# Performance work log

Hardware: AMD Instinct MI355X
Metric: run time of the kernel (lower is better)

Reference implementation:

```python
import jax, jax.numpy as jnp
import numpy as np

EPS = 1e-6

def rms_norm(x):
    # x / sqrt(mean(x^2, axis=-1) + eps)
    return x * jax.lax.rsqrt(jnp.mean(x * x, axis=-1, keepdims=True) + EPS)

def setup_inputs() -> dict:
    key = jax.random.key(0)
    k1, k2, k3 = jax.random.split(key, 3)
    T, B, D = 2048, 16, 1024
    x = jax.random.normal(k1, (T, B, D), dtype=jnp.float32)
    h0 = jax.random.normal(k2, (B, D), dtype=jnp.float32)
    # Orthogonal-ish init scaled by 0.5 (faithful to nn.init.orthogonal_ then *0.5)
    A = jax.random.normal(k3, (D, D), dtype=jnp.float32)
    Q, _ = jnp.linalg.qr(A)
    W = 0.5 * Q
    b = jnp.zeros((D,), dtype=jnp.float32)
    log_alpha = jnp.asarray(np.log(0.1), dtype=jnp.float32)
    return {"x": x, "h0": h0, "W": W, "b": b, "log_alpha": log_alpha}

def reference(x, h0, W, b, log_alpha):
    T, B, D = x.shape
    alpha = jnp.exp(log_alpha)
    # Precompute Wx for all timesteps: [T, B, D]
    Wx_all = jnp.einsum('tbd,ed->tbe', x, W) + b

    def step(h_prev, wx_t):
        h_raw = h_prev + alpha * wx_t
        h_new = rms_norm(h_raw)
        out = h_new * jax.nn.silu(h_new)
        return h_new, (h_new, out)

    _, (h_seq, output) = jax.lax.scan(step, h0, Wx_all)
    h = jnp.concatenate([h0[None], h_seq], axis=0)  # [T+1, B, D]
    return output, h
```

## Files before the change

### kernel.cpp

```cpp
#include <hip/hip_runtime.h>
#include <hip/hip_bf16.h>

#define TT 2048
#define BB 16
#define DD 1024
#define BD (BB*DD)
#define MR (TT*BB)
#define EPSV 1e-6f
#define INVD (1.0f/1024.0f)
#define CH 256
#define NCH (TT/CH)
#define RING 8

typedef __bf16 bf16x8_t __attribute__((ext_vector_type(8)));
typedef float  f32x4_t  __attribute__((ext_vector_type(4)));
typedef __attribute__((address_space(1))) void gvoid_t;
typedef __attribute__((address_space(3))) void lvoid_t;

static __device__ __forceinline__ float wave_red_sum(float ss) {
    asm volatile(
        "s_nop 1\n\t"
        "v_add_f32 %0, %0, %0 row_shr:1 bound_ctrl:0\n\t"
        "s_nop 1\n\t"
        "v_add_f32 %0, %0, %0 row_shr:2 bound_ctrl:0\n\t"
        "s_nop 1\n\t"
        "v_add_f32 %0, %0, %0 row_shr:4 bank_mask:0xe\n\t"
        "s_nop 1\n\t"
        "v_add_f32 %0, %0, %0 row_shr:8 bank_mask:0xc\n\t"
        "s_nop 1\n\t"
        "v_add_f32 %0, %0, %0 row_bcast:15 row_mask:0xa\n\t"
        "s_nop 1\n\t"
        "v_add_f32 %0, %0, %0 row_bcast:31 row_mask:0xc\n\t"
        "s_nop 1"
        : "+v"(ss));
    return __builtin_bit_cast(float, __builtin_amdgcn_readlane(__builtin_bit_cast(int, ss), 63));
}

static __device__ __forceinline__ unsigned short f2bf(float f) {
    __hip_bfloat16 h = __float2bfloat16(f);
    return __builtin_bit_cast(unsigned short, h);
}

__global__ void k_convert(const float* __restrict__ x, const float* __restrict__ W,
                          unsigned short* __restrict__ xb, unsigned short* __restrict__ wb) {
    const long NX4 = (long)MR * DD / 4;
    const long NW4 = (long)DD * DD / 4;
    const long stride = (long)gridDim.x * blockDim.x;
    for (long j = (long)blockIdx.x * blockDim.x + threadIdx.x; j < NX4 + NW4; j += stride) {
        const float4* src; unsigned short* dst; long o;
        if (j < NX4) { src = (const float4*)x; dst = xb; o = j; }
        else         { src = (const float4*)W; dst = wb; o = j - NX4; }
        float4 v = src[o];
        ushort4 u;
        u.x = f2bf(v.x); u.y = f2bf(v.y); u.z = f2bf(v.z); u.w = f2bf(v.w);
        *(ushort4*)(dst + o * 4) = u;
    }
}

__global__ __launch_bounds__(256, 2)
void k_gemm(const unsigned short* __restrict__ A, const unsigned short* __restrict__ Bw,
            const float* __restrict__ bias, float* __restrict__ C) {
    __shared__ char lds[16384];
    char* ldsA = lds;
    char* ldsB = lds + 8192;
    const int tid  = threadIdx.x;
    const int lane = tid & 63;
    const int wid  = tid >> 6;
    const int wm = wid >> 1, wn = wid & 1;
    const size_t arow0 = (size_t)blockIdx.y * 128;
    const int    brow0 = blockIdx.x * 128;

    f32x4_t acc[4][4] = {};

    const int off0 = tid * 16,        row0_ = off0 >> 6, colb0 = off0 & 63;
    const int off1 = 4096 + tid * 16, row1_ = off1 >> 6, colb1 = off1 & 63;

    for (int kk = 0; kk < DD / 32; ++kk) {
        const int kbase = kk * 32;
        __builtin_amdgcn_global_load_lds(
            (gvoid_t*)(A + (arow0 + row0_) * DD + kbase + (colb0 >> 1)),
            (lvoid_t*)(ldsA + off0), 16, 0, 0);
        __builtin_amdgcn_global_load_lds(
            (gvoid_t*)(A + (arow0 + row1_) * DD + kbase + (colb1 >> 1)),
            (lvoid_t*)(ldsA + off1), 16, 0, 0);
        __builtin_amdgcn_global_load_lds(
            (gvoid_t*)(Bw + (size_t)(brow0 + row0_) * DD + kbase + (colb0 >> 1)),
            (lvoid_t*)(ldsB + off0), 16, 0, 0);
        __builtin_amdgcn_global_load_lds(
            (gvoid_t*)(Bw + (size_t)(brow0 + row1_) * DD + kbase + (colb1 >> 1)),
            (lvoid_t*)(ldsB + off1), 16, 0, 0);
        __syncthreads();

        const int ml = lane & 15;
        const int kh = (lane >> 4) * 16;
        bf16x8_t av[4], bv[4];
        #pragma unroll
        for (int i = 0; i < 4; ++i) {
            av[i] = *(const bf16x8_t*)(ldsA + (wm * 64 + i * 16 + ml) * 64 + kh);
            bv[i] = *(const bf16x8_t*)(ldsB + (wn * 64 + i * 16 + ml) * 64 + kh);
        }
        #pragma unroll
        for (int i = 0; i < 4; ++i)
            #pragma unroll
            for (int j = 0; j < 4; ++j)
                acc[i][j] = __builtin_amdgcn_mfma_f32_16x16x32_bf16(av[i], bv[j], acc[i][j], 0, 0, 0);
        __syncthreads();
    }

    const int rq = (lane >> 4) * 4;
    const int cl = lane & 15;
    #pragma unroll
    for (int i = 0; i < 4; ++i) {
        #pragma unroll
        for (int j = 0; j < 4; ++j) {
            const int n = brow0 + wn * 64 + j * 16 + cl;
            const float bb = bias[n];
            #pragma unroll
            for (int q = 0; q < 4; ++q) {
                const size_t m = arow0 + wm * 64 + i * 16 + rq + q;
                C[m * DD + n] = acc[i][j][q] + bb;
            }
        }
    }
}

__global__ __launch_bounds__(64, 1)
void k_phaseA(const float* __restrict__ Wx, const float* __restrict__ h0,
              const float* __restrict__ la, float* __restrict__ hout,
              float* __restrict__ rtab) {
    const int b = blockIdx.x;
    const int lane = threadIdx.x;
    const int dof = lane * 4;
    const float alpha = expf(la[0]);
    const float* wbase = Wx + b * DD + dof;

    float h[16];
    #pragma unroll
    for (int k = 0; k < 4; ++k) {
        float4 v = *(const float4*)(h0 + b * DD + k * 256 + dof);
        h[k*4+0] = v.x; h[k*4+1] = v.y; h[k*4+2] = v.z; h[k*4+3] = v.w;
    }
    asm volatile("" :: "v"(h[0]), "v"(h[1]), "v"(h[2]), "v"(h[3]),
                       "v"(h[4]), "v"(h[5]), "v"(h[6]), "v"(h[7]),
                       "v"(h[8]), "v"(h[9]), "v"(h[10]), "v"(h[11]),
                       "v"(h[12]), "v"(h[13]), "v"(h[14]), "v"(h[15]));
    __builtin_amdgcn_sched_barrier(0);

    f32x4_t buf[RING][4];
    #pragma unroll
    for (int s = 0; s < RING; ++s) {
        const float* wp = wbase + (size_t)s * BD;
        #pragma unroll
        for (int k = 0; k < 4; ++k)
            asm volatile("global_load_dwordx4 %0, %1, off"
                         : "=v"(buf[s][k]) : "v"(wp + k * 256));
    }

    float r_keep = 0.f;

    for (int tt = 0; tt < TT; tt += 8) {
        #pragma unroll
        for (int g = 0; g < 2; ++g) {
            const int m0 = tt + g * 4;

            asm volatile("s_waitcnt vmcnt(16)" ::: "memory");
            __builtin_amdgcn_sched_barrier(0);

            if ((m0 & 255) == 0) {
                float* hp = hout + (size_t)m0 * BD + b * DD;
                #pragma unroll
                for (int k = 0; k < 4; ++k) {
                    float4 v; v.x = h[k*4+0]; v.y = h[k*4+1];
                    v.z = h[k*4+2]; v.w = h[k*4+3];
                    *(float4*)(hp + k * 256 + dof) = v;
                }
            }

            #pragma unroll
            for (int s4 = 0; s4 < 4; ++s4) {
                const int s = g * 4 + s4;
                const int m = m0 + s4;
                float hr[16];
                float p0 = 0.f, p1 = 0.f, p2 = 0.f, p3 = 0.f;
                #pragma unroll
                for (int k = 0; k < 4; ++k) {
                    const f32x4_t w = buf[s][k];
                    hr[k*4+0] = fmaf(alpha, w[0], h[k*4+0]);
                    hr[k*4+1] = fmaf(alpha, w[1], h[k*4+1]);
                    hr[k*4+2] = fmaf(alpha, w[2], h[k*4+2]);
                    hr[k*4+3] = fmaf(alpha, w[3], h[k*4+3]);
                    p0 = fmaf(hr[k*4+0], hr[k*4+0], p0);
                    p1 = fmaf(hr[k*4+1], hr[k*4+1], p1);
                    p2 = fmaf(hr[k*4+2], hr[k*4+2], p2);
                    p3 = fmaf(hr[k*4+3], hr[k*4+3], p3);
                }
                const float total = wave_red_sum((p0 + p1) + (p2 + p3));
                const float rt = __builtin_amdgcn_rsqf(fmaf(total, INVD, EPSV));
                r_keep = (lane == (m & 63)) ? rt : r_keep;
                #pragma unroll
                for (int e = 0; e < 16; ++e) h[e] = rt * hr[e];
            }

            if (g == 1 && (tt & 63) == 56)
                rtab[(size_t)b * TT + (tt - 56) + lane] = r_keep;

            #pragma unroll
            for (int s4 = 0; s4 < 4; ++s4) {
                const int s = g * 4 + s4;
                const float* wp = wbase + (size_t)((m0 + 8 + s4) & (TT - 1)) * BD;
                #pragma unroll
                for (int k = 0; k < 4; ++k)
                    asm volatile("global_load_dwordx4 %0, %1, off"
                                 : "=v"(buf[s][k]) : "v"(wp + k * 256));
            }
        }
    }

    asm volatile("s_waitcnt vmcnt(0)" ::: "memory");
}

__global__ __launch_bounds__(256)
void k_phaseB(float* __restrict__ WxOut, float* __restrict__ hout,
              const float* __restrict__ rtab, const float* __restrict__ la) {
    const int col = blockIdx.x * 256 + threadIdx.x;
    const int c = blockIdx.y;
    const int b = col >> 10;
    const float alpha = expf(la[0]);
    const float* rr = rtab + b * TT;
    float h = hout[(size_t)(c * CH) * BD + col];
    const int t0 = c * CH + 1;
    float w = WxOut[(size_t)(t0 - 1) * BD + col];
    for (int s = 0; s < CH; ++s) {
        const int t = t0 + s;
        float wnext = 0.f;
        if (s + 1 < CH) wnext = WxOut[(size_t)t * BD + col];
        const float r = rr[t - 1];
        const float hraw = fmaf(alpha, w, h);
        const float hn = r * hraw;
        const float sg = 1.0f / (1.0f + __expf(-hn));
        WxOut[(size_t)(t - 1) * BD + col] = hn * hn * sg;
        if ((t & (CH - 1)) != 0 || t == TT)
            hout[(size_t)t * BD + col] = hn;
        h = hn;
        w = wnext;
    }
}

extern "C" void kernel_launch(void* const* d_in, const int* in_sizes, int n_in,
                              void* d_out, int out_size, void* d_ws, size_t ws_size,
                              hipStream_t stream) {
    (void)in_sizes; (void)n_in; (void)out_size; (void)ws_size;
    const float* x    = (const float*)d_in[0];
    const float* h0   = (const float*)d_in[1];
    const float* W    = (const float*)d_in[2];
    const float* bias = (const float*)d_in[3];
    const float* la   = (const float*)d_in[4];

    float* outr = (float*)d_out;
    float* hreg = outr + (size_t)TT * BD;
    unsigned short* xb = (unsigned short*)hreg;
    unsigned short* wb = xb + (size_t)MR * DD;
    float* rtab = (float*)d_ws;

    k_convert<<<2048, 256, 0, stream>>>(x, W, xb, wb);
    k_gemm<<<dim3(DD / 128, MR / 128), 256, 0, stream>>>(xb, wb, bias, outr);
    k_phaseA<<<BB, 64, 0, stream>>>(outr, h0, la, hreg, rtab);
    k_phaseB<<<dim3(BD / 256, NCH), 256, 0, stream>>>(outr, hreg, rtab, la);
}
```

Measured before the change: 512.4 us.

## Fuse GEMM, sequential scan and output pass into one persistent kernel with counters

Combines the GEMM, the per-batch sequential RMS-norm scan and the chunked output pass into a single launch whose blocks pick roles by block id. Atomic row-tile counters let the scan start as soon as the GEMM rows it needs are written, and per-batch progress flags let output chunks start while the scan continues. The scan and early GEMM tiles get raised wave priority. This adds spin-waits and relies on all scan blocks being resident and making forward progress, and it moves the bf16 staging buffers so they do not overlap the live h region.

Result: slower. 880.3 us (+71.8%).

```diff
diff --git a/kernel.cpp b/kernel.cpp
--- a/kernel.cpp
+++ b/kernel.cpp
@@ -11,6 +11,10 @@
 #define CH 256
 #define NCH (TT/CH)
 #define RING 8
+
+#define ID_GEMM   16
+#define ID_PB     2064
+#define ID_END    2576
 
 typedef __bf16 bf16x8_t __attribute__((ext_vector_type(8)));
 typedef float  f32x4_t  __attribute__((ext_vector_type(4)));
@@ -58,198 +62,237 @@
 }
 
 __global__ __launch_bounds__(256, 2)
-void k_gemm(const unsigned short* __restrict__ A, const unsigned short* __restrict__ Bw,
-            const float* __restrict__ bias, float* __restrict__ C) {
+void k_mega(const unsigned short* __restrict__ A, const unsigned short* __restrict__ Bw,
+            const float* __restrict__ bias, float* __restrict__ outr,
+            const float* __restrict__ h0, const float* __restrict__ la,
+            float* __restrict__ hreg, float* __restrict__ rtab,
+            int* cnt, int* prog, int role_base, int gated) {
     __shared__ char lds[16384];
-    char* ldsA = lds;
-    char* ldsB = lds + 8192;
-    const int tid  = threadIdx.x;
-    const int lane = tid & 63;
-    const int wid  = tid >> 6;
-    const int wm = wid >> 1, wn = wid & 1;
-    const size_t arow0 = (size_t)blockIdx.y * 128;
-    const int    brow0 = blockIdx.x * 128;
-
-    f32x4_t acc[4][4] = {};
-
-    const int off0 = tid * 16,        row0_ = off0 >> 6, colb0 = off0 & 63;
-    const int off1 = 4096 + tid * 16, row1_ = off1 >> 6, colb1 = off1 & 63;
-
-    for (int kk = 0; kk < DD / 32; ++kk) {
-        const int kbase = kk * 32;
-        __builtin_amdgcn_global_load_lds(
-            (gvoid_t*)(A + (arow0 + row0_) * DD + kbase + (colb0 >> 1)),
-            (lvoid_t*)(ldsA + off0), 16, 0, 0);
-        __builtin_amdgcn_global_load_lds(
-            (gvoid_t*)(A + (arow0 + row1_) * DD + kbase + (colb1 >> 1)),
-            (lvoid_t*)(ldsA + off1), 16, 0, 0);
-        __builtin_amdgcn_global_load_lds(
-            (gvoid_t*)(Bw + (size_t)(brow0 + row0_) * DD + kbase + (colb0 >> 1)),
-            (lvoid_t*)(ldsB + off0), 16, 0, 0);
-        __builtin_amdgcn_global_load_lds(
-            (gvoid_t*)(Bw + (size_t)(brow0 + row1_) * DD + kbase + (colb1 >> 1)),
-            (lvoid_t*)(ldsB + off1), 16, 0, 0);
-        __syncthreads();
-
-        const int ml = lane & 15;
-        const int kh = (lane >> 4) * 16;
-        bf16x8_t av[4], bv[4];
+    const int id = blockIdx.x + role_base;
+    const int tid = threadIdx.x;
+
+    if (id >= ID_GEMM && id < ID_PB) {
+        const int gid = id - ID_GEMM;
+        const int gx = gid & 7, gy = gid >> 3;
+        if (gated && gy < 64) __builtin_amdgcn_s_setprio(1);
+        char* ldsA = lds;
+        char* ldsB = lds + 8192;
+        const int lane = tid & 63;
+        const int wid  = tid >> 6;
+        const int wm = wid >> 1, wn = wid & 1;
+        const size_t arow0 = (size_t)gy * 128;
+        const int    brow0 = gx * 128;
+
+        f32x4_t acc[4][4] = {};
+        const int off0 = tid * 16,        row0_ = off0 >> 6, colb0 = off0 & 63;
+        const int off1 = 4096 + tid * 16, row1_ = off1 >> 6, colb1 = off1 & 63;
+
+        for (int kk = 0; kk < DD / 32; ++kk) {
+            const int kbase = kk * 32;
+            __builtin_amdgcn_global_load_lds(
+                (gvoid_t*)(A + (arow0 + row0_) * DD + kbase + (colb0 >> 1)),
+                (lvoid_t*)(ldsA + off0), 16, 0, 0);
+            __builtin_amdgcn_global_load_lds(
+                (gvoid_t*)(A + (arow0 + row1_) * DD + kbase + (colb1 >> 1)),
+                (lvoid_t*)(ldsA + off1), 16, 0, 0);
+            __builtin_amdgcn_global_load_lds(
+                (gvoid_t*)(Bw + (size_t)(brow0 + row0_) * DD + kbase + (colb0 >> 1)),
+                (lvoid_t*)(ldsB + off0), 16, 0, 0);
+            __builtin_amdgcn_global_load_lds(
+                (gvoid_t*)(Bw + (size_t)(brow0 + row1_) * DD + kbase + (colb1 >> 1)),
+                (lvoid_t*)(ldsB + off1), 16, 0, 0);
+            __syncthreads();
+
+            const int ml = lane & 15;
+            const int kh = (lane >> 4) * 16;
+            bf16x8_t av[4], bv[4];
+            #pragma unroll
+            for (int i = 0; i < 4; ++i) {
+                av[i] = *(const bf16x8_t*)(ldsA + (wm * 64 + i * 16 + ml) * 64 + kh);
+                bv[i] = *(const bf16x8_t*)(ldsB + (wn * 64 + i * 16 + ml) * 64 + kh);
+            }
+            #pragma unroll
+            for (int i = 0; i < 4; ++i)
+                #pragma unroll
+                for (int j = 0; j < 4; ++j)
+                    acc[i][j] = __builtin_amdgcn_mfma_f32_16x16x32_bf16(av[i], bv[j], acc[i][j], 0, 0, 0);
+            __syncthreads();
+        }
+
+        const int rq = (lane >> 4) * 4;
+        const int cl = lane & 15;
         #pragma unroll
         for (int i = 0; i < 4; ++i) {
-            av[i] = *(const bf16x8_t*)(ldsA + (wm * 64 + i * 16 + ml) * 64 + kh);
-            bv[i] = *(const bf16x8_t*)(ldsB + (wn * 64 + i * 16 + ml) * 64 + kh);
-        }
+            #pragma unroll
+            for (int j = 0; j < 4; ++j) {
+                const int n = brow0 + wn * 64 + j * 16 + cl;
+                const float bb = bias[n];
+                #pragma unroll
+                for (int q = 0; q < 4; ++q) {
+                    const size_t m = arow0 + wm * 64 + i * 16 + rq + q;
+                    outr[m * DD + n] = acc[i][j][q] + bb;
+                }
+            }
+        }
+        if (gated) {
+            __syncthreads();
+            if (tid == 0)
+                __hip_atomic_fetch_add(&cnt[gy], 1, __ATOMIC_RELEASE,
+                                       __HIP_MEMORY_SCOPE_AGENT);
+        }
+        return;
+    }
+
+    if (id < ID_GEMM) {
+        const int b = id;
+        if (tid >= 64) return;
+        const int lane = tid;
+        const int dof = lane * 4;
+        const float alpha = expf(la[0]);
+        const float* wbase = outr + b * DD + dof;
+        __builtin_amdgcn_s_setprio(1);
+
+        float h[16];
         #pragma unroll
-        for (int i = 0; i < 4; ++i)
-            #pragma unroll
-            for (int j = 0; j < 4; ++j)
-                acc[i][j] = __builtin_amdgcn_mfma_f32_16x16x32_bf16(av[i], bv[j], acc[i][j], 0, 0, 0);
-        __syncthreads();
-    }
-
-    const int rq = (lane >> 4) * 4;
-    const int cl = lane & 15;
-    #pragma unroll
-    for (int i = 0; i < 4; ++i) {
+        for (int k = 0; k < 4; ++k) {
+            float4 v = *(const float4*)(h0 + b * DD + k * 256 + dof);
+            h[k*4+0] = v.x; h[k*4+1] = v.y; h[k*4+2] = v.z; h[k*4+3] = v.w;
+        }
+        asm volatile("" :: "v"(h[0]), "v"(h[1]), "v"(h[2]), "v"(h[3]),
+                           "v"(h[4]), "v"(h[5]), "v"(h[6]), "v"(h[7]),
+                           "v"(h[8]), "v"(h[9]), "v"(h[10]), "v"(h[11]),
+                           "v"(h[12]), "v"(h[13]), "v"(h[14]), "v"(h[15]));
+        __builtin_amdgcn_sched_barrier(0);
+
+        if (gated && lane == 0) {
+            while (__hip_atomic_load(&cnt[0], __ATOMIC_ACQUIRE,
+                                     __HIP_MEMORY_SCOPE_AGENT) < 8)
+                __builtin_amdgcn_s_sleep(8);
+        }
+
+        f32x4_t buf[RING][4];
         #pragma unroll
-        for (int j = 0; j < 4; ++j) {
-            const int n = brow0 + wn * 64 + j * 16 + cl;
-            const float bb = bias[n];
-            #pragma unroll
-            for (int q = 0; q < 4; ++q) {
-                const size_t m = arow0 + wm * 64 + i * 16 + rq + q;
-                C[m * DD + n] = acc[i][j][q] + bb;
-            }
-        }
-    }
-}
-
-__global__ __launch_bounds__(64, 1)
-void k_phaseA(const float* __restrict__ Wx, const float* __restrict__ h0,
-              const float* __restrict__ la, float* __restrict__ hout,
-              float* __restrict__ rtab) {
-    const int b = blockIdx.x;
-    const int lane = threadIdx.x;
-    const int dof = lane * 4;
-    const float alpha = expf(la[0]);
-    const float* wbase = Wx + b * DD + dof;
-
-    float h[16];
-    #pragma unroll
-    for (int k = 0; k < 4; ++k) {
-        float4 v = *(const float4*)(h0 + b * DD + k * 256 + dof);
-        h[k*4+0] = v.x; h[k*4+1] = v.y; h[k*4+2] = v.z; h[k*4+3] = v.w;
-    }
-    asm volatile("" :: "v"(h[0]), "v"(h[1]), "v"(h[2]), "v"(h[3]),
-                       "v"(h[4]), "v"(h[5]), "v"(h[6]), "v"(h[7]),
-                       "v"(h[8]), "v"(h[9]), "v"(h[10]), "v"(h[11]),
-                       "v"(h[12]), "v"(h[13]), "v"(h[14]), "v"(h[15]));
-    __builtin_amdgcn_sched_barrier(0);
-
-    f32x4_t buf[RING][4];
-    #pragma unroll
-    for (int s = 0; s < RING; ++s) {
-        const float* wp = wbase + (size_t)s * BD;
-        #pragma unroll
-        for (int k = 0; k < 4; ++k)
-            asm volatile("global_load_dwordx4 %0, %1, off"
-                         : "=v"(buf[s][k]) : "v"(wp + k * 256));
-    }
-
-    float r_keep = 0.f;
-
-    for (int tt = 0; tt < TT; tt += 8) {
-        #pragma unroll
-        for (int g = 0; g < 2; ++g) {
-            const int m0 = tt + g * 4;
-
-            asm volatile("s_waitcnt vmcnt(16)" ::: "memory");
-            __builtin_amdgcn_sched_barrier(0);
-
-            if ((m0 & 255) == 0) {
-                float* hp = hout + (size_t)m0 * BD + b * DD;
+        for (int s = 0; s < RING; ++s) {
+            const float* wp = wbase + (size_t)s * BD;
+            #pragma unroll
+            for (int k = 0; k < 4; ++k)
+                asm volatile("global_load_dwordx4 %0, %1, off"
+                             : "=v"(buf[s][k]) : "v"(wp + k * 256));
+        }
+
+        float r_keep = 0.f;
+
+        for (int tt = 0; tt < TT; tt += 8) {
+            if (gated && lane == 0) {
+                int y = (tt >> 3) + 1; if (y > 255) y = 255;
+                while (__hip_atomic_load(&cnt[y], __ATOMIC_ACQUIRE,
+                                         __HIP_MEMORY_SCOPE_AGENT) < 8)
+                    __builtin_amdgcn_s_sleep(8);
+            }
+            #pragma unroll
+            for (int g = 0; g < 2; ++g) {
+                const int m0 = tt + g * 4;
+
+                asm volatile("s_waitcnt vmcnt(16)" ::: "memory");
+                __builtin_amdgcn_sched_barrier(0);
+
+                if ((m0 & 255) == 0) {
+                    float* hp = hreg + (size_t)m0 * BD + b * DD;
+                    #pragma unroll
+                    for (int k = 0; k < 4; ++k) {
+                        float4 v; v.x = h[k*4+0]; v.y = h[k*4+1];
+                        v.z = h[k*4+2]; v.w = h[k*4+3];
+                        *(float4*)(hp + k * 256 + dof) = v;
+                    }
+                }
+
                 #pragma unroll
-                for (int k = 0; k < 4; ++k) {
-                    float4 v; v.x = h[k*4+0]; v.y = h[k*4+1];
-                    v.z = h[k*4+2]; v.w = h[k*4+3];
-                    *(float4*)(hp + k * 256 + dof) = v;
+                for (int s4 = 0; s4 < 4; ++s4) {
+                    const int s = g * 4 + s4;
+                    const int m = m0 + s4;
+                    float hr[16];
+                    float p0 = 0.f, p1 = 0.f, p2 = 0.f, p3 = 0.f;
+                    #pragma unroll
+                    for (int k = 0; k < 4; ++k) {
+                        const f32x4_t w = buf[s][k];
+                        hr[k*4+0] = fmaf(alpha, w[0], h[k*4+0]);
+                        hr[k*4+1] = fmaf(alpha, w[1], h[k*4+1]);
+                        hr[k*4+2] = fmaf(alpha, w[2], h[k*4+2]);
+                        hr[k*4+3] = fmaf(alpha, w[3], h[k*4+3]);
+                        p0 = fmaf(hr[k*4+0], hr[k*4+0], p0);
+                        p1 = fmaf(hr[k*4+1], hr[k*4+1], p1);
+                        p2 = fmaf(hr[k*4+2], hr[k*4+2], p2);
+                        p3 = fmaf(hr[k*4+3], hr[k*4+3], p3);
+                    }
+                    const float total = wave_red_sum((p0 + p1) + (p2 + p3));
+                    const float rt = __builtin_amdgcn_rsqf(fmaf(total, INVD, EPSV));
+                    r_keep = (lane == (m & 63)) ? rt : r_keep;
+                    #pragma unroll
+                    for (int e = 0; e < 16; ++e) h[e] = rt * hr[e];
                 }
-            }
-
-            #pragma unroll
-            for (int s4 = 0; s4 < 4; ++s4) {
-                const int s = g * 4 + s4;
-                const int m = m0 + s4;
-                float hr[16];
-                float p0 = 0.f, p1 = 0.f, p2 = 0.f, p3 = 0.f;
+
+                if (g == 1 && (tt & 63) == 56)
+                    rtab[(size_t)b * TT + (tt - 56) + lane] = r_keep;
+
                 #pragma unroll
-                for (int k = 0; k < 4; ++k) {
-                    const f32x4_t w = buf[s][k];
-                    hr[k*4+0] = fmaf(alpha, w[0], h[k*4+0]);
-                    hr[k*4+1] = fmaf(alpha, w[1], h[k*4+1]);
-                    hr[k*4+2] = fmaf(alpha, w[2], h[k*4+2]);
-                    hr[k*4+3] = fmaf(alpha, w[3], h[k*4+3]);
-                    p0 = fmaf(hr[k*4+0], hr[k*4+0], p0);
-                    p1 = fmaf(hr[k*4+1], hr[k*4+1], p1);
-                    p2 = fmaf(hr[k*4+2], hr[k*4+2], p2);
-                    p3 = fmaf(hr[k*4+3], hr[k*4+3], p3);
+                for (int s4 = 0; s4 < 4; ++s4) {
+                    const int s = g * 4 + s4;
+                    const float* wp = wbase + (size_t)((m0 + 8 + s4) & (TT - 1)) * BD;
+                    #pragma unroll
+                    for (int k = 0; k < 4; ++k)
+                        asm volatile("global_load_dwordx4 %0, %1, off"
+                                     : "=v"(buf[s][k]) : "v"(wp + k * 256));
                 }
-                const float total = wave_red_sum((p0 + p1) + (p2 + p3));
-                const float rt = __builtin_amdgcn_rsqf(fmaf(total, INVD, EPSV));
-                r_keep = (lane == (m & 63)) ? rt : r_keep;
-                #pragma unroll
-                for (int e = 0; e < 16; ++e) h[e] = rt * hr[e];
-            }
-
-            if (g == 1 && (tt & 63) == 56)
-                rtab[(size_t)b * TT + (tt - 56) + lane] = r_keep;
-
-            #pragma unroll
-            for (int s4 = 0; s4 < 4; ++s4) {
-                const int s = g * 4 + s4;
-                const float* wp = wbase + (size_t)((m0 + 8 + s4) & (TT - 1)) * BD;
-                #pragma unroll
-                for (int k = 0; k < 4; ++k)
-                    asm volatile("global_load_dwordx4 %0, %1, off"
-                                 : "=v"(buf[s][k]) : "v"(wp + k * 256));
-            }
-        }
-    }
-
-    asm volatile("s_waitcnt vmcnt(0)" ::: "memory");
-}
-
-__global__ __launch_bounds__(256)
-void k_phaseB(float* __restrict__ WxOut, float* __restrict__ hout,
-              const float* __restrict__ rtab, const float* __restrict__ la) {
-    const int col = blockIdx.x * 256 + threadIdx.x;
-    const int c = blockIdx.y;
-    const int b = col >> 10;
-    const float alpha = expf(la[0]);
-    const float* rr = rtab + b * TT;
-    float h = hout[(size_t)(c * CH) * BD + col];
-    const int t0 = c * CH + 1;
-    float w = WxOut[(size_t)(t0 - 1) * BD + col];
-    for (int s = 0; s < CH; ++s) {
-        const int t = t0 + s;
-        float wnext = 0.f;
-        if (s + 1 < CH) wnext = WxOut[(size_t)t * BD + col];
-        const float r = rr[t - 1];
-        const float hraw = fmaf(alpha, w, h);
-        const float hn = r * hraw;
-        const float sg = 1.0f / (1.0f + __expf(-hn));
-        WxOut[(size_t)(t - 1) * BD + col] = hn * hn * sg;
-        if ((t & (CH - 1)) != 0 || t == TT)
-            hout[(size_t)t * BD + col] = hn;
-        h = hn;
-        w = wnext;
+            }
+
+            if (gated && (tt & 255) == 248 && lane == 0) {
+                __hip_atomic_store(&prog[b], (tt + 8) >> 8, __ATOMIC_RELEASE,
+                                   __HIP_MEMORY_SCOPE_AGENT);
+            }
+        }
+        asm volatile("s_waitcnt vmcnt(0)" ::: "memory");
+        return;
+    }
+
+    {
+        const int pid = id - ID_PB;
+        const int c = pid >> 6;
+        const int col = (pid & 63) * 256 + tid;
+        const int b = col >> 10;
+        if (gated) {
+            if (tid == 0) {
+                while (__hip_atomic_load(&prog[b], __ATOMIC_ACQUIRE,
+                                         __HIP_MEMORY_SCOPE_AGENT) < c + 1)
+                    __builtin_amdgcn_s_sleep(64);
+            }
+            __syncthreads();
+        }
+        const float alpha = expf(la[0]);
+        const float* rr = rtab + b * TT;
+        float h = hreg[(size_t)(c * CH) * BD + col];
+        const int t0 = c * CH + 1;
+        float w = outr[(size_t)(t0 - 1) * BD + col];
+        for (int s = 0; s < CH; ++s) {
+            const int t = t0 + s;
+            float wnext = 0.f;
+            if (s + 1 < CH) wnext = outr[(size_t)t * BD + col];
+            const float r = rr[t - 1];
+            const float hraw = fmaf(alpha, w, h);
+            const float hn = r * hraw;
+            const float sg = 1.0f / (1.0f + __expf(-hn));
+            outr[(size_t)(t - 1) * BD + col] = hn * hn * sg;
+            if ((t & (CH - 1)) != 0 || t == TT)
+                hreg[(size_t)t * BD + col] = hn;
+            h = hn;
+            w = wnext;
+        }
     }
 }
 
 extern "C" void kernel_launch(void* const* d_in, const int* in_sizes, int n_in,
                               void* d_out, int out_size, void* d_ws, size_t ws_size,
                               hipStream_t stream) {
-    (void)in_sizes; (void)n_in; (void)out_size; (void)ws_size;
+    (void)in_sizes; (void)n_in; (void)out_size;
     const float* x    = (const float*)d_in[0];
     const float* h0   = (const float*)d_in[1];
     const float* W    = (const float*)d_in[2];
@@ -258,12 +301,25 @@
 
     float* outr = (float*)d_out;
     float* hreg = outr + (size_t)TT * BD;
-    unsigned short* xb = (unsigned short*)hreg;
+    unsigned short* xb = (unsigned short*)(hreg + (size_t)993 * BD);
     unsigned short* wb = xb + (size_t)MR * DD;
     float* rtab = (float*)d_ws;
+    int*   cnt  = (int*)d_ws + (size_t)TT * BB;
+    int*   prog = cnt + 256;
+    const size_t need = (size_t)TT * BB * 4 + (256 + 16) * 4;
+    const bool fused = ws_size >= need;
 
     k_convert<<<2048, 256, 0, stream>>>(x, W, xb, wb);
-    k_gemm<<<dim3(DD / 128, MR / 128), 256, 0, stream>>>(xb, wb, bias, outr);
-    k_phaseA<<<BB, 64, 0, stream>>>(outr, h0, la, hreg, rtab);
-    k_phaseB<<<dim3(BD / 256, NCH), 256, 0, stream>>>(outr, hreg, rtab, la);
-}
+    if (fused) {
+        hipMemsetAsync(cnt, 0, (256 + 16) * sizeof(int), stream);
+        k_mega<<<ID_END, 256, 0, stream>>>(xb, wb, bias, outr, h0, la,
+                                           hreg, rtab, cnt, prog, 0, 1);
+    } else {
+        k_mega<<<2048, 256, 0, stream>>>(xb, wb, bias, outr, h0, la,
+                                         hreg, rtab, nullptr, nullptr, ID_GEMM, 0);
+        k_mega<<<16, 256, 0, stream>>>(xb, wb, bias, outr, h0, la,
+                                       hreg, rtab, nullptr, nullptr, 0, 0);
+        k_mega<<<512, 256, 0, stream>>>(xb, wb, bias, outr, h0, la,
+                                        hreg, rtab, nullptr, nullptr, ID_PB, 0);
+    }
+}
```
